# Kernel tuning notes

Measured on AMD Instinct MI355X. Metric: run time of the kernel, lower is better.

## Reference

```python
import jax, jax.numpy as jnp
import numpy as np


def setup_inputs() -> dict:
    key = jax.random.key(0)
    ks = jax.random.split(key, 6)
    B, T, D, U = 32, 2048, 512, 512
    scale = 1.0 / np.sqrt(D)
    return {
        "values": jax.random.normal(ks[0], (B, T, D), dtype=jnp.float32),
        "query": jax.random.normal(ks[1], (B, D), dtype=jnp.float32),
        "W1": jax.random.normal(ks[2], (D, U), dtype=jnp.float32) * scale,
        "b1": jnp.zeros((U,), dtype=jnp.float32),
        "W2": jax.random.normal(ks[3], (D, U), dtype=jnp.float32) * scale,
        "b2": jnp.zeros((U,), dtype=jnp.float32),
        "V": jax.random.normal(ks[4], (U, 1), dtype=jnp.float32) * (1.0 / np.sqrt(U)),
        "bV": jnp.zeros((1,), dtype=jnp.float32),
    }


def reference(values, query, W1, b1, W2, b2, V, bV):
    # values: [B,T,D], query: [B,D]
    proj_v = jnp.einsum("btd,du->btu", values, W1) + b1          # [B,T,U]
    proj_q = (query @ W2 + b2)[:, None, :]                        # [B,1,U]
    score = jnp.tanh(proj_v + proj_q) @ V + bV                    # [B,T,1]
    attention_weights = jax.nn.softmax(score, axis=1)             # [B,T,1]
    context_vector = jnp.sum(attention_weights * values, axis=1)  # [B,D]
    return context_vector, attention_weights
```

## Files before the change

### kernel.cpp

```cpp
#include <hip/hip_runtime.h>
#include <math.h>


#define B_ 32
#define T_ 2048
#define D_ 512
#define U_ 512
#define M_ (B_ * T_)

typedef _Float16 half8 __attribute__((ext_vector_type(8)));
typedef float floatx4 __attribute__((ext_vector_type(4)));

__device__ __forceinline__ float fast_tanh(float x) {
  x = fminf(fmaxf(x, -20.f), 20.f);
  const float e = __expf(2.f * x);
  return 1.f - 2.f / (e + 1.f);
}

__device__ __forceinline__ void load_lds16f(const float* g, float* l) {
  __builtin_amdgcn_global_load_lds(
      (const __attribute__((address_space(1))) void*)g,
      (__attribute__((address_space(3))) void*)l, 16, 0, 0);
}

__device__ __forceinline__ void load_lds16h(const _Float16* g, _Float16* l) {
  __builtin_amdgcn_global_load_lds(
      (const __attribute__((address_space(1))) void*)g,
      (__attribute__((address_space(3))) void*)l, 16, 0, 0);
}

__global__ __launch_bounds__(256) void prep_fused(
    const float* __restrict__ W1, const float* __restrict__ query,
    const float* __restrict__ W2, const float* __restrict__ b2,
    _Float16* __restrict__ w1t, float* __restrict__ projq,
    float* __restrict__ context) {
  __shared__ float sh[64 * 65];
  const int bx = blockIdx.x;
  const int tid = threadIdx.x;
  if (bx < 64) {
    const int t = bx;
    const int k0 = (t >> 3) * 64, u0 = (t & 7) * 64;
    float(*sm)[65] = (float(*)[65])sh;
    const int lu = tid & 63;
    const int g = tid >> 6;
#pragma unroll
    for (int i = 0; i < 16; ++i) {
      const int row = g * 16 + i;
      sm[row][lu] = W1[(long)(k0 + row) * U_ + u0 + lu];
    }
    __syncthreads();
#pragma unroll
    for (int i = 0; i < 16; ++i) {
      const int row = g * 16 + i;
      w1t[(long)(u0 + row) * D_ + k0 + lu] = (_Float16)sm[lu][row];
    }
  } else {
    const int t = bx - 64;
    const int gid = t * 256 + tid;
    context[gid] = 0.f;
    const int b = t >> 1;
    const int u = (t & 1) * 256 + tid;
    for (int d = tid; d < D_; d += 256) sh[d] = query[b * D_ + d];
    __syncthreads();
    float acc = 0.f;
#pragma unroll 8
    for (int d = 0; d < D_; ++d) acc += sh[d] * W2[d * U_ + u];
    projq[b * U_ + u] = acc + b2[u];
  }
}

__global__ __launch_bounds__(512, 1) void score_fused(
    const float* __restrict__ values, const _Float16* __restrict__ w1t,
    const float* __restrict__ b1, const float* __restrict__ projq,
    const float* __restrict__ V, float* __restrict__ scores) {
  const int m0 = blockIdx.x * 128;
  const int b = blockIdx.x >> 4;
  const int tid = threadIdx.x;
  const int lane = tid & 63;
  const int w = tid >> 6;
  const int wm = (w & 1) * 64;
  const int wu = (w >> 1) * 128;
  const int ln = lane & 15;
  const int lq = lane >> 4;

  __shared__ alignas(16) float As[2][128 * 32];
  __shared__ alignas(16) _Float16 Bs[2][512 * 32];
  __shared__ float red[4][128];

  const int dr = lane >> 3;
  const int dc = (lane & 7) ^ dr;
  const float* gA[2];
#pragma unroll
  for (int j = 0; j < 2; ++j) {
    const int r = w * 16 + j * 8 + dr;
    gA[j] = values + (long)(m0 + r) * D_ + dc * 4;
  }

  const int br = lane >> 2;
  const int bc = (lane & 3) ^ (br & 3);
  const _Float16* gB[4];
#pragma unroll
  for (int i = 0; i < 4; ++i) {
    const int r = w * 64 + i * 16 + br;
    gB[i] = w1t + (long)r * D_ + bc * 8;
  }

  floatx4 acc[4][8] = {};

#pragma unroll
  for (int j = 0; j < 2; ++j)
    load_lds16f(gA[j], &As[0][(w * 16 + j * 8) * 32]);
#pragma unroll
  for (int i = 0; i < 4; ++i)
    load_lds16h(gB[i], &Bs[0][(w * 64 + i * 16) * 32]);
  __syncthreads();

  for (int t = 0; t < 16; ++t) {
    const int p = t & 1;
    if (t < 15) {
#pragma unroll
      for (int j = 0; j < 2; ++j)
        load_lds16f(gA[j] + (t + 1) * 32, &As[p ^ 1][(w * 16 + j * 8) * 32]);
#pragma unroll
      for (int i = 0; i < 4; ++i)
        load_lds16h(gB[i] + (t + 1) * 32, &Bs[p ^ 1][(w * 64 + i * 16) * 32]);
    }
    half8 bf[8];
#pragma unroll
    for (int ni = 0; ni < 8; ++ni) {
      const int r = wu + ni * 16 + ln;
      bf[ni] = *(const half8*)&Bs[p][r * 32 + ((lq ^ (ln & 3)) * 8)];
    }
    half8 af[4];
#pragma unroll
    for (int mi = 0; mi < 4; ++mi) {
      const int r = wm + mi * 16 + ln;
      const float* row = &As[p][r * 32];
      const float4 lo = *(const float4*)(row + (((2 * lq) ^ (r & 7)) * 4));
      const float4 hi = *(const float4*)(row + (((2 * lq + 1) ^ (r & 7)) * 4));
      af[mi] = half8{(_Float16)lo.x, (_Float16)lo.y, (_Float16)lo.z,
                     (_Float16)lo.w, (_Float16)hi.x, (_Float16)hi.y,
                     (_Float16)hi.z, (_Float16)hi.w};
    }
#pragma unroll
    for (int mi = 0; mi < 4; ++mi)
#pragma unroll
      for (int ni = 0; ni < 8; ++ni)
        acc[mi][ni] = __builtin_amdgcn_mfma_f32_16x16x32_f16(
            af[mi], bf[ni], acc[mi][ni], 0, 0, 0);
    __syncthreads();
  }

  float pre[8], vv[8];
#pragma unroll
  for (int ni = 0; ni < 8; ++ni) {
    const int u = wu + ni * 16 + ln;
    pre[ni] = b1[u] + projq[b * U_ + u];
    vv[ni] = V[u];
  }
#pragma unroll
  for (int mi = 0; mi < 4; ++mi) {
#pragma unroll
    for (int r = 0; r < 4; ++r) {
      float t = 0.f;
#pragma unroll
      for (int ni = 0; ni < 8; ++ni)
        t += fast_tanh(acc[mi][ni][r] + pre[ni]) * vv[ni];
      t += __shfl_xor(t, 1);
      t += __shfl_xor(t, 2);
      t += __shfl_xor(t, 4);
      t += __shfl_xor(t, 8);
      if (ln == 0) red[w >> 1][wm + mi * 16 + lq * 4 + r] = t;
    }
  }
  __syncthreads();
  if (tid < 128)
    scores[m0 + tid] =
        red[0][tid] + red[1][tid] + red[2][tid] + red[3][tid];
}

__global__ __launch_bounds__(256) void softmax_context_kernel(
    const float* __restrict__ scores, const float* __restrict__ values,
    float* __restrict__ weights, float* __restrict__ context) {
  const int b = blockIdx.x;
  const int t0 = blockIdx.y * 128;
  const int tid = threadIdx.x;

  float v[8];
  float mx = -INFINITY;
#pragma unroll
  for (int i = 0; i < 8; ++i) {
    v[i] = scores[b * T_ + i * 256 + tid];
    mx = fmaxf(mx, v[i]);
  }
#pragma unroll
  for (int off = 32; off > 0; off >>= 1) mx = fmaxf(mx, __shfl_down(mx, off));
  __shared__ float sm[4], ss[4];
  if ((tid & 63) == 0) sm[tid >> 6] = mx;
  __syncthreads();
  mx = fmaxf(fmaxf(sm[0], sm[1]), fmaxf(sm[2], sm[3]));
  float sum = 0.f;
#pragma unroll
  for (int i = 0; i < 8; ++i) sum += __expf(v[i] - mx);
#pragma unroll
  for (int off = 32; off > 0; off >>= 1) sum += __shfl_down(sum, off);
  if ((tid & 63) == 0) ss[tid >> 6] = sum;
  __syncthreads();
  const float inv = 1.f / (ss[0] + ss[1] + ss[2] + ss[3]);

  __shared__ float wsh[128];
  if (tid < 128) {
    const float ww = __expf(scores[b * T_ + t0 + tid] - mx) * inv;
    wsh[tid] = ww;
    weights[b * T_ + t0 + tid] = ww;
  }
  __syncthreads();

  const int g = tid >> 7;
  const int dx = tid & 127;
  __shared__ float4 part[128];
  float4 acc = make_float4(0.f, 0.f, 0.f, 0.f);
  const float4* vp = (const float4*)(values + (long)(b * T_ + t0 + g) * D_) + dx;
#pragma unroll 8
  for (int t = 0; t < 64; ++t) {
    const float4 x = vp[(long)(2 * t) * (D_ / 4)];
    const float ww = wsh[2 * t + g];
    acc.x += ww * x.x; acc.y += ww * x.y; acc.z += ww * x.z; acc.w += ww * x.w;
  }
  if (g == 0) part[dx] = acc;
  __syncthreads();
  if (g == 1) {
    const float4 p = part[dx];
    atomicAdd(&context[b * D_ + dx * 4 + 0], acc.x + p.x);
    atomicAdd(&context[b * D_ + dx * 4 + 1], acc.y + p.y);
    atomicAdd(&context[b * D_ + dx * 4 + 2], acc.z + p.z);
    atomicAdd(&context[b * D_ + dx * 4 + 3], acc.w + p.w);
  }
}

extern "C" void kernel_launch(void* const* d_in, const int* in_sizes, int n_in,
                              void* d_out, int out_size, void* d_ws, size_t ws_size,
                              hipStream_t stream) {
  const float* values = (const float*)d_in[0];
  const float* query = (const float*)d_in[1];
  const float* W1 = (const float*)d_in[2];
  const float* b1 = (const float*)d_in[3];
  const float* W2 = (const float*)d_in[4];
  const float* b2 = (const float*)d_in[5];
  const float* V = (const float*)d_in[6];

  float* out = (float*)d_out;
  float* context = out;
  float* weights = out + B_ * D_;
  float* projq = (float*)d_ws;
  float* scores = projq + B_ * U_;
  _Float16* w1t = (_Float16*)((char*)d_ws + 65536 + 262144);

  prep_fused<<<128, 256, 0, stream>>>(W1, query, W2, b2, w1t, projq, context);
  score_fused<<<M_ / 128, 512, 0, stream>>>(values, w1t, b1, projq, V, scores);
  softmax_context_kernel<<<dim3(B_, T_ / 128), 256, 0, stream>>>(
      scores, values, weights, context);
}
```

Measured before the change: 298.9 us.

## Fuse softmax-weighted context into score kernel via online-softmax partials

```diff
diff --git a/kernel.cpp b/kernel.cpp
--- a/kernel.cpp
+++ b/kernel.cpp
@@ -32,8 +32,7 @@
 __global__ __launch_bounds__(256) void prep_fused(
     const float* __restrict__ W1, const float* __restrict__ query,
     const float* __restrict__ W2, const float* __restrict__ b2,
-    _Float16* __restrict__ w1t, float* __restrict__ projq,
-    float* __restrict__ context) {
+    _Float16* __restrict__ w1t, float* __restrict__ projq) {
   __shared__ float sh[64 * 65];
   const int bx = blockIdx.x;
   const int tid = threadIdx.x;
@@ -56,8 +55,6 @@
     }
   } else {
     const int t = bx - 64;
-    const int gid = t * 256 + tid;
-    context[gid] = 0.f;
     const int b = t >> 1;
     const int u = (t & 1) * 256 + tid;
     for (int d = tid; d < D_; d += 256) sh[d] = query[b * D_ + d];
@@ -72,7 +69,8 @@
 __global__ __launch_bounds__(512, 1) void score_fused(
     const float* __restrict__ values, const _Float16* __restrict__ w1t,
     const float* __restrict__ b1, const float* __restrict__ projq,
-    const float* __restrict__ V, float* __restrict__ scores) {
+    const float* __restrict__ V, float* __restrict__ scores,
+    float* __restrict__ cpart, float* __restrict__ pms) {
   const int m0 = blockIdx.x * 128;
   const int b = blockIdx.x >> 4;
   const int tid = threadIdx.x;
@@ -86,6 +84,8 @@
   __shared__ alignas(16) float As[2][128 * 32];
   __shared__ alignas(16) _Float16 Bs[2][512 * 32];
   __shared__ float red[4][128];
+  __shared__ float sc[128], ev[128];
+  __shared__ float4 part[512];
 
   const int dr = lane >> 3;
   const int dc = (lane & 7) ^ dr;
@@ -174,67 +174,85 @@
     }
   }
   __syncthreads();
-  if (tid < 128)
-    scores[m0 + tid] =
-        red[0][tid] + red[1][tid] + red[2][tid] + red[3][tid];
-}
-
-__global__ __launch_bounds__(256) void softmax_context_kernel(
-    const float* __restrict__ scores, const float* __restrict__ values,
-    float* __restrict__ weights, float* __restrict__ context) {
-  const int b = blockIdx.x;
-  const int t0 = blockIdx.y * 128;
-  const int tid = threadIdx.x;
-
-  float v[8];
-  float mx = -INFINITY;
-#pragma unroll
-  for (int i = 0; i < 8; ++i) {
-    v[i] = scores[b * T_ + i * 256 + tid];
-    mx = fmaxf(mx, v[i]);
-  }
-#pragma unroll
-  for (int off = 32; off > 0; off >>= 1) mx = fmaxf(mx, __shfl_down(mx, off));
-  __shared__ float sm[4], ss[4];
-  if ((tid & 63) == 0) sm[tid >> 6] = mx;
-  __syncthreads();
-  mx = fmaxf(fmaxf(sm[0], sm[1]), fmaxf(sm[2], sm[3]));
-  float sum = 0.f;
-#pragma unroll
-  for (int i = 0; i < 8; ++i) sum += __expf(v[i] - mx);
-#pragma unroll
-  for (int off = 32; off > 0; off >>= 1) sum += __shfl_down(sum, off);
-  if ((tid & 63) == 0) ss[tid >> 6] = sum;
-  __syncthreads();
-  const float inv = 1.f / (ss[0] + ss[1] + ss[2] + ss[3]);
-
-  __shared__ float wsh[128];
   if (tid < 128) {
-    const float ww = __expf(scores[b * T_ + t0 + tid] - mx) * inv;
-    wsh[tid] = ww;
-    weights[b * T_ + t0 + tid] = ww;
-  }
-  __syncthreads();
+    const float s = red[0][tid] + red[1][tid] + red[2][tid] + red[3][tid];
+    scores[m0 + tid] = s;
+    sc[tid] = s;
+  }
+  __syncthreads();
+
+  float m = -INFINITY;
+#pragma unroll 8
+  for (int i = 0; i < 128; ++i) m = fmaxf(m, sc[i]);
+  if (tid < 128) ev[tid] = __expf(sc[tid] - m);
+  __syncthreads();
+  float S = 0.f;
+#pragma unroll 8
+  for (int i = 0; i < 128; ++i) S += ev[i];
 
   const int g = tid >> 7;
   const int dx = tid & 127;
-  __shared__ float4 part[128];
-  float4 acc = make_float4(0.f, 0.f, 0.f, 0.f);
-  const float4* vp = (const float4*)(values + (long)(b * T_ + t0 + g) * D_) + dx;
-#pragma unroll 8
-  for (int t = 0; t < 64; ++t) {
-    const float4 x = vp[(long)(2 * t) * (D_ / 4)];
-    const float ww = wsh[2 * t + g];
-    acc.x += ww * x.x; acc.y += ww * x.y; acc.z += ww * x.z; acc.w += ww * x.w;
-  }
-  if (g == 0) part[dx] = acc;
-  __syncthreads();
-  if (g == 1) {
-    const float4 p = part[dx];
-    atomicAdd(&context[b * D_ + dx * 4 + 0], acc.x + p.x);
-    atomicAdd(&context[b * D_ + dx * 4 + 1], acc.y + p.y);
-    atomicAdd(&context[b * D_ + dx * 4 + 2], acc.z + p.z);
-    atomicAdd(&context[b * D_ + dx * 4 + 3], acc.w + p.w);
+  float4 a4 = make_float4(0.f, 0.f, 0.f, 0.f);
+  const float4* vp = (const float4*)(values + (long)(m0 + g) * D_) + dx;
+#pragma unroll 8
+  for (int i = 0; i < 32; ++i) {
+    const float4 x = vp[(long)(4 * i) * (D_ / 4)];
+    const float wgt = ev[4 * i + g];
+    a4.x += wgt * x.x; a4.y += wgt * x.y; a4.z += wgt * x.z; a4.w += wgt * x.w;
+  }
+  part[tid] = a4;
+  __syncthreads();
+  if (tid < 128) {
+    const float4 p0 = part[dx], p1 = part[dx + 128];
+    const float4 p2 = part[dx + 256], p3 = part[dx + 384];
+    float4 tot;
+    tot.x = p0.x + p1.x + p2.x + p3.x;
+    tot.y = p0.y + p1.y + p2.y + p3.y;
+    tot.z = p0.z + p1.z + p2.z + p3.z;
+    tot.w = p0.w + p1.w + p2.w + p3.w;
+    *(float4*)&cpart[(long)blockIdx.x * D_ + dx * 4] = tot;
+  }
+  if (tid == 0) {
+    pms[blockIdx.x * 2 + 0] = m;
+    pms[blockIdx.x * 2 + 1] = S;
+  }
+}
+
+__global__ __launch_bounds__(256) void finalize_kernel(
+    const float* __restrict__ scores, const float* __restrict__ cpart,
+    const float* __restrict__ pms, float* __restrict__ weights,
+    float* __restrict__ context) {
+  const int b = blockIdx.x;
+  const int tid = threadIdx.x;
+  __shared__ float sM[16], sS[16];
+  if (tid < 16) {
+    sM[tid] = pms[(b * 16 + tid) * 2 + 0];
+    sS[tid] = pms[(b * 16 + tid) * 2 + 1];
+  }
+  __syncthreads();
+  float M = -INFINITY;
+#pragma unroll
+  for (int j = 0; j < 16; ++j) M = fmaxf(M, sM[j]);
+  float denom = 0.f;
+#pragma unroll
+  for (int j = 0; j < 16; ++j) denom += __expf(sM[j] - M) * sS[j];
+  const float inv = 1.f / denom;
+
+  float c0 = 0.f, c1 = 0.f;
+#pragma unroll
+  for (int j = 0; j < 16; ++j) {
+    const float f = __expf(sM[j] - M);
+    const float2 cc = *(const float2*)&cpart[(long)(b * 16 + j) * D_ + tid * 2];
+    c0 += f * cc.x;
+    c1 += f * cc.y;
+  }
+  context[b * D_ + tid * 2 + 0] = c0 * inv;
+  context[b * D_ + tid * 2 + 1] = c1 * inv;
+
+#pragma unroll
+  for (int i = 0; i < 8; ++i) {
+    const int t = i * 256 + tid;
+    weights[b * T_ + t] = __expf(scores[b * T_ + t] - M) * inv;
   }
 }
 
@@ -255,9 +273,12 @@
   float* projq = (float*)d_ws;
   float* scores = projq + B_ * U_;
   _Float16* w1t = (_Float16*)((char*)d_ws + 65536 + 262144);
-
-  prep_fused<<<128, 256, 0, stream>>>(W1, query, W2, b2, w1t, projq, context);
-  score_fused<<<M_ / 128, 512, 0, stream>>>(values, w1t, b1, projq, V, scores);
-  softmax_context_kernel<<<dim3(B_, T_ / 128), 256, 0, stream>>>(
-      scores, values, weights, context);
-}
+  float* cpart = (float*)((char*)d_ws + 851968);
+  float* pms = (float*)((char*)d_ws + 851968 + 1048576);
+
+  prep_fused<<<128, 256, 0, stream>>>(W1, query, W2, b2, w1t, projq);
+  score_fused<<<M_ / 128, 512, 0, stream>>>(values, w1t, b1, projq, V, scores,
+                                            cpart, pms);
+  finalize_kernel<<<B_, 256, 0, stream>>>(scores, cpart, pms, weights,
+                                          context);
+}
```

Result: no change. 302.7 us (+1.3%).
